# Kernel optimization log

Hardware: AMD Instinct MI355X
Metric: run time of the kernel (lower is better)

Reference implementation:

```python
import jax, jax.numpy as jnp
import numpy as np

BLOCK = 32          # per_1x32 microscaling block size along K
FP4_MAX = 6.0       # largest magnitude representable in e2m1
FP4_EMAX = 2.0      # exponent of largest fp4 binade (4..6)


def _quant_dequant_mxfp4(x):
    """Simulate MXFP4 (e2m1 elements, shared power-of-two E8M0 scale per 1x32
    block along the last dim): quantize then dequantize. x: [..., K], K % 32 == 0."""
    shape = x.shape
    xb = x.reshape(*shape[:-1], shape[-1] // BLOCK, BLOCK)
    amax = jnp.max(jnp.abs(xb), axis=-1, keepdims=True)
    # shared scale: 2^(floor(log2(amax)) - emax) so the block max lands in the top binade
    exp = jnp.floor(jnp.log2(jnp.maximum(amax, jnp.finfo(x.dtype).tiny))) - FP4_EMAX
    scale = jnp.where(amax > 0, jnp.exp2(exp), jnp.ones_like(amax))
    q = jnp.clip(xb / scale, -FP4_MAX, FP4_MAX)
    aq = jnp.abs(q)
    # e2m1 ulp: 0.5 on [0,2), 1 on [2,4), 2 on [4,6]
    lsb = jnp.where(aq < 2.0, 0.5, jnp.where(aq < 4.0, 1.0, 2.0))
    qr = jnp.round(q / lsb) * lsb  # round-to-nearest-even onto the fp4 grid
    return (qr * scale).reshape(shape)


def setup_inputs() -> dict:
    key = jax.random.key(0)
    k1, k2, k3 = jax.random.split(key, 3)
    B, S, K, N = 4, 2048, 2048, 2048
    inp = jax.random.normal(k1, (B, S, K), dtype=jnp.float32)
    weight = jax.random.normal(k2, (N, K), dtype=jnp.float32) * (1.0 / np.sqrt(K))
    bias = jax.random.normal(k3, (N,), dtype=jnp.float32) * 0.02
    return {"input": inp, "weight": weight, "bias": bias}


def reference(input, weight, bias):
    # both activation and weight are fake-quantized to MXFP4 per 1x32 blocks
    # along the contraction (in_features) dim, then a standard GEMM + bias.
    orig_shape = input.shape
    a = _quant_dequant_mxfp4(input.reshape(-1, orig_shape[-1]))  # [M, K]
    w = _quant_dequant_mxfp4(weight)                              # [N, K]
    out = jnp.einsum("mk,nk->mn", a, w) + bias
    return out.reshape(*orig_shape[:-1], weight.shape[0])
```

## Files before the change

### kernel.cpp

```cpp
#include <hip/hip_runtime.h>
#include <cstdint>


#define BM 128
#define BN 128
#define BK 128

typedef float floatx4 __attribute__((ext_vector_type(4)));
typedef int intx8 __attribute__((ext_vector_type(8)));

#define GLOBAL_AS __attribute__((address_space(1)))
#define LDS_AS __attribute__((address_space(3)))


__device__ __forceinline__ int enc1(float x, float inv) {
    float q = x * inv;
    q = fminf(fmaxf(q, -6.0f), 6.0f);
    int s = (int)(__float_as_uint(q) >> 31) << 3;
    float aq = fabsf(q);
    float ilsb = aq < 2.0f ? 2.0f : (aq < 4.0f ? 1.0f : 0.5f);
    float lsb  = aq < 2.0f ? 0.5f : (aq < 4.0f ? 1.0f : 2.0f);
    float ar = rintf(aq * ilsb) * lsb;
    int c;
    if (ar < 2.0f)      c = (int)(ar * 2.0f);
    else if (ar < 4.0f) c = 2 + (int)ar;
    else                c = 4 + (int)(ar * 0.5f);
    return c | s;
}

__global__ void quant_mxfp4_v4(const float* __restrict__ A, uint8_t* __restrict__ Aq,
                               uint8_t* __restrict__ AscT,
                               const float* __restrict__ W, uint8_t* __restrict__ Wq,
                               uint8_t* __restrict__ WscT,
                               long na4, long ntot4, int s4, long Mr, long Nr) {
    long t = (long)blockIdx.x * 256 + threadIdx.x;
    if (t >= ntot4) return;
    const float* src; uint8_t* dq; uint8_t* ds; long idx; long rows;
    if (t < na4) { src = A; dq = Aq; ds = AscT; idx = t; rows = Mr; }
    else         { src = W; dq = Wq; ds = WscT; idx = t - na4; rows = Nr; }

    float4 f = ((const float4*)src)[idx];
    float amax = fmaxf(fmaxf(fabsf(f.x), fabsf(f.y)),
                       fmaxf(fabsf(f.z), fabsf(f.w)));
    amax = fmaxf(amax, __shfl_xor(amax, 1));
    amax = fmaxf(amax, __shfl_xor(amax, 2));
    amax = fmaxf(amax, __shfl_xor(amax, 4));

    int ebits = (int)((__float_as_uint(amax) >> 23) & 0xff);
    int sb;
    float inv;
    if (amax > 0.0f) {
        sb = ebits - 2; if (sb < 0) sb = 0;
        inv = __uint_as_float((unsigned)((256 - ebits) & 255) << 23);
    } else {
        sb = 127;
        inv = 0.0f;
    }

    int c0 = enc1(f.x, inv), c1 = enc1(f.y, inv);
    int c2 = enc1(f.z, inv), c3 = enc1(f.w, inv);
    ((unsigned short*)dq)[idx] =
        (unsigned short)(c0 | (c1 << 4) | (c2 << 8) | (c3 << 12));
    if ((idx & 7) == 0) {
        long m  = idx >> s4;
        int  kb = (int)((idx & ((1L << s4) - 1)) >> 3);
        ds[(size_t)kb * rows + m] = (uint8_t)sb;
    }
}


__global__ __launch_bounds__(256, 4) void gemm_fp4_v4(
        const uint8_t* __restrict__ Aq, const uint8_t* __restrict__ AscT,
        const uint8_t* __restrict__ Wq, const uint8_t* __restrict__ WscT,
        const float* __restrict__ bias, float* __restrict__ C,
        int M, int N, int K) {
    __shared__ __align__(16) uint8_t sA[2][BM * 64];
    __shared__ __align__(16) uint8_t sB[2][BN * 64];
    __shared__ __align__(16) uint8_t sSA[2][4 * 128];
    __shared__ __align__(16) uint8_t sSB[2][4 * 128];

    const int tid = threadIdx.x;
    const int lane = tid & 63;
    const int w = tid >> 6;
    const int wr = w >> 1;
    const int wc = w & 1;
    const int row16 = lane & 15;
    const int quad = lane >> 4;

    const int id = blockIdx.x;
    const int g = id & 7, h = id >> 3;
    const int by = g + 8 * (h & 7);
    const int bx = h >> 3;
    const int m0 = by * BM;
    const int n0 = bx * BN;
    const int KB2 = K >> 1;
    const int NT = K / BK;

    const int rA = wr * 64 + row16;
    const int rB = wc * 64 + row16;

    floatx4 acc[4][4];
#pragma unroll
    for (int i = 0; i < 4; i++)
#pragma unroll
        for (int j = 0; j < 4; j++) acc[i][j] = (floatx4){0.f, 0.f, 0.f, 0.f};

    auto stage = [&](int tt) {
        const int bb = tt & 1;
        const int kb = tt * 64;
#pragma unroll
        for (int it = 0; it < 2; ++it) {
            int idx = it * 256 + tid;
            int row = idx >> 2, c = idx & 3;
            const uint8_t* src = Aq + (size_t)(m0 + row) * KB2 + kb + c * 16;
            __builtin_amdgcn_global_load_lds((GLOBAL_AS void*)src,
                (LDS_AS void*)(&sA[bb][idx * 16]), 16, 0, 0);
        }
#pragma unroll
        for (int it = 0; it < 2; ++it) {
            int idx = it * 256 + tid;
            int row = idx >> 2, c = idx & 3;
            const uint8_t* src = Wq + (size_t)(n0 + row) * KB2 + kb + c * 16;
            __builtin_amdgcn_global_load_lds((GLOBAL_AS void*)src,
                (LDS_AS void*)(&sB[bb][idx * 16]), 16, 0, 0);
        }
        if (tid < 128) {
            int kbi = tid >> 5, moff = (tid & 31) * 4;
            const uint8_t* src = AscT + (size_t)(4 * tt + kbi) * M + m0 + moff;
            __builtin_amdgcn_global_load_lds((GLOBAL_AS void*)src,
                (LDS_AS void*)(&sSA[bb][tid * 4]), 4, 0, 0);
        } else {
            int tw = tid - 128;
            int kbi = tw >> 5, noff = (tw & 31) * 4;
            const uint8_t* src = WscT + (size_t)(4 * tt + kbi) * N + n0 + noff;
            __builtin_amdgcn_global_load_lds((GLOBAL_AS void*)src,
                (LDS_AS void*)(&sSB[bb][tw * 4]), 4, 0, 0);
        }
    };

    stage(0);
    stage(1);
    asm volatile("s_waitcnt vmcnt(5)" ::: "memory");
    __builtin_amdgcn_sched_barrier(0);
    __builtin_amdgcn_s_barrier();

    for (int t = 0; t < NT; ++t) {
        const int p = t & 1;
        const uint8_t* pa = sA[p];
        const uint8_t* pb = sB[p];

        int4 afr[4], bfr[4];
        int sab[4], swb[4];
#pragma unroll
        for (int ni = 0; ni < 4; ++ni) {
            int r = rB + ni * 16;
            bfr[ni] = *(const int4*)(pb + r * 64 + quad * 16);
            swb[ni] = (int)sSB[p][quad * 128 + wc * 64 + ni * 16 + row16];
        }
#pragma unroll
        for (int mi = 0; mi < 4; ++mi) {
            int r = rA + mi * 16;
            afr[mi] = *(const int4*)(pa + r * 64 + quad * 16);
            sab[mi] = (int)sSA[p][quad * 128 + wr * 64 + mi * 16 + row16];
        }

        asm volatile("s_waitcnt lgkmcnt(0)" ::: "memory");
        __builtin_amdgcn_sched_barrier(0);
        __builtin_amdgcn_s_barrier();

        if (t + 2 < NT) stage(t + 2);

        __builtin_amdgcn_s_setprio(1);
#pragma unroll
        for (int mi = 0; mi < 4; ++mi) {
            intx8 a8 = {afr[mi].x, afr[mi].y, afr[mi].z, afr[mi].w, 0, 0, 0, 0};
#pragma unroll
            for (int ni = 0; ni < 4; ++ni) {
                intx8 b8 = {bfr[ni].x, bfr[ni].y, bfr[ni].z, bfr[ni].w, 0, 0, 0, 0};
                acc[mi][ni] = __builtin_amdgcn_mfma_scale_f32_16x16x128_f8f6f4(
                    a8, b8, acc[mi][ni], 4, 4, 0, sab[mi], 0, swb[ni]);
            }
        }
        __builtin_amdgcn_s_setprio(0);

        if (t < NT - 1) {
            if (t + 2 < NT) asm volatile("s_waitcnt vmcnt(5)" ::: "memory");
            else            asm volatile("s_waitcnt vmcnt(0)" ::: "memory");
            __builtin_amdgcn_sched_barrier(0);
            __builtin_amdgcn_s_barrier();
        }
    }

#pragma unroll
    for (int ni = 0; ni < 4; ++ni) {
        int n = n0 + wc * 64 + ni * 16 + row16;
        float bv = bias[n];
#pragma unroll
        for (int mi = 0; mi < 4; ++mi) {
            int mbase = m0 + wr * 64 + mi * 16 + quad * 4;
#pragma unroll
            for (int r = 0; r < 4; ++r) {
                C[(size_t)(mbase + r) * N + n] = acc[mi][ni][r] + bv;
            }
        }
    }
}


extern "C" void kernel_launch(void* const* d_in, const int* in_sizes, int n_in,
                              void* d_out, int out_size, void* d_ws, size_t ws_size,
                              hipStream_t stream) {
    const float* inp  = (const float*)d_in[0];
    const float* wgt  = (const float*)d_in[1];
    const float* bias = (const float*)d_in[2];
    float* out = (float*)d_out;

    const int N = in_sizes[2];
    const int K = in_sizes[1] / N;
    const long M = (long)in_sizes[0] / K;

    uint8_t* Aq4  = (uint8_t*)d_ws;
    uint8_t* Wq4  = Aq4 + (size_t)M * K / 2;
    uint8_t* AscT = Wq4 + (size_t)N * K / 2;
    uint8_t* WscT = AscT + (size_t)M * K / 32;

    int s4 = 0;
    while ((1 << s4) < (K >> 2)) ++s4;

    long na4   = (long)M * K / 4;
    long ntot4 = na4 + (long)N * K / 4;
    quant_mxfp4_v4<<<dim3((ntot4 + 255) / 256), dim3(256), 0, stream>>>(
        inp, Aq4, AscT, wgt, Wq4, WscT, na4, ntot4, s4, M, (long)N);

    dim3 grid((N / BN) * (int)(M / BM));
    gemm_fp4_v4<<<grid, dim3(256), 0, stream>>>(
        Aq4, AscT, Wq4, WscT, bias, out, (int)M, N, K);
}
```

Before: 156.7 us.

## Enlarge GEMM tile to 256x128 with 512 threads, triple-buffer LDS, split-phase loads

The FP4 GEMM moves from a 128x128 to a 256x128 block tile with 8 waves, and from double to triple LDS buffering. Each k-step is split into two MFMA phases, each preceded by its own A-fragment reads, and the prefetch of tile t+2 is split so A is issued in the first phase and B plus scales in the second, interleaving global-to-LDS loads with compute. This halves the grid and increases reuse of each B tile. In exchange it adds extra barriers per iteration, raises LDS use per block, which may lower occupancy, and reworks the block-index swizzle for the new grid shape.

```diff
diff --git a/kernel.cpp b/kernel.cpp
--- a/kernel.cpp
+++ b/kernel.cpp
@@ -2,9 +2,10 @@
 #include <cstdint>
 
 
-#define BM 128
+#define BM 256
 #define BN 128
 #define BK 128
+#define NBUF 3
 
 typedef float floatx4 __attribute__((ext_vector_type(4)));
 typedef int intx8 __attribute__((ext_vector_type(8)));
@@ -69,15 +70,15 @@
 }
 
 
-__global__ __launch_bounds__(256, 4) void gemm_fp4_v4(
+__global__ __launch_bounds__(512, 4) void gemm_fp4_v5(
         const uint8_t* __restrict__ Aq, const uint8_t* __restrict__ AscT,
         const uint8_t* __restrict__ Wq, const uint8_t* __restrict__ WscT,
         const float* __restrict__ bias, float* __restrict__ C,
         int M, int N, int K) {
-    __shared__ __align__(16) uint8_t sA[2][BM * 64];
-    __shared__ __align__(16) uint8_t sB[2][BN * 64];
-    __shared__ __align__(16) uint8_t sSA[2][4 * 128];
-    __shared__ __align__(16) uint8_t sSB[2][4 * 128];
+    __shared__ __align__(16) uint8_t sA[NBUF][BM * 64];
+    __shared__ __align__(16) uint8_t sB[NBUF][BN * 64];
+    __shared__ __align__(16) uint8_t sSA[NBUF][4 * BM];
+    __shared__ __align__(16) uint8_t sSB[NBUF][4 * BN];
 
     const int tid = threadIdx.x;
     const int lane = tid & 63;
@@ -89,8 +90,8 @@
 
     const int id = blockIdx.x;
     const int g = id & 7, h = id >> 3;
-    const int by = g + 8 * (h & 7);
-    const int bx = h >> 3;
+    const int by = g + 8 * (h & 3);
+    const int bx = h >> 2;
     const int m0 = by * BM;
     const int n0 = bx * BN;
     const int KB2 = K >> 1;
@@ -105,74 +106,76 @@
 #pragma unroll
         for (int j = 0; j < 4; j++) acc[i][j] = (floatx4){0.f, 0.f, 0.f, 0.f};
 
-    auto stage = [&](int tt) {
-        const int bb = tt & 1;
+    auto stageA = [&](int tt) {
+        const int bb = tt % NBUF;
         const int kb = tt * 64;
 #pragma unroll
         for (int it = 0; it < 2; ++it) {
-            int idx = it * 256 + tid;
+            int idx = it * 512 + tid;
             int row = idx >> 2, c = idx & 3;
             const uint8_t* src = Aq + (size_t)(m0 + row) * KB2 + kb + c * 16;
             __builtin_amdgcn_global_load_lds((GLOBAL_AS void*)src,
                 (LDS_AS void*)(&sA[bb][idx * 16]), 16, 0, 0);
         }
-#pragma unroll
-        for (int it = 0; it < 2; ++it) {
-            int idx = it * 256 + tid;
-            int row = idx >> 2, c = idx & 3;
+    };
+    auto stageB = [&](int tt) {
+        const int bb = tt % NBUF;
+        const int kb = tt * 64;
+        {
+            int row = tid >> 2, c = tid & 3;
             const uint8_t* src = Wq + (size_t)(n0 + row) * KB2 + kb + c * 16;
             __builtin_amdgcn_global_load_lds((GLOBAL_AS void*)src,
-                (LDS_AS void*)(&sB[bb][idx * 16]), 16, 0, 0);
-        }
-        if (tid < 128) {
-            int kbi = tid >> 5, moff = (tid & 31) * 4;
+                (LDS_AS void*)(&sB[bb][tid * 16]), 16, 0, 0);
+        }
+        if (tid >= 256) {
+            int local = tid - 256;
+            int kbi = local >> 6, moff = (local & 63) * 4;
             const uint8_t* src = AscT + (size_t)(4 * tt + kbi) * M + m0 + moff;
             __builtin_amdgcn_global_load_lds((GLOBAL_AS void*)src,
-                (LDS_AS void*)(&sSA[bb][tid * 4]), 4, 0, 0);
-        } else {
-            int tw = tid - 128;
-            int kbi = tw >> 5, noff = (tw & 31) * 4;
+                (LDS_AS void*)(&sSA[bb][local * 4]), 4, 0, 0);
+        } else if (tid < 128) {
+            int kbi = tid >> 5, noff = (tid & 31) * 4;
             const uint8_t* src = WscT + (size_t)(4 * tt + kbi) * N + n0 + noff;
             __builtin_amdgcn_global_load_lds((GLOBAL_AS void*)src,
-                (LDS_AS void*)(&sSB[bb][tw * 4]), 4, 0, 0);
+                (LDS_AS void*)(&sSB[bb][tid * 4]), 4, 0, 0);
         }
     };
 
-    stage(0);
-    stage(1);
-    asm volatile("s_waitcnt vmcnt(5)" ::: "memory");
+    stageA(0); stageB(0);
+    if (NT > 1) { stageA(1); stageB(1); }
+    if (NT > 1) asm volatile("s_waitcnt vmcnt(3)" ::: "memory");
+    else        asm volatile("s_waitcnt vmcnt(0)" ::: "memory");
     __builtin_amdgcn_sched_barrier(0);
     __builtin_amdgcn_s_barrier();
 
     for (int t = 0; t < NT; ++t) {
-        const int p = t & 1;
+        const int p = t % NBUF;
         const uint8_t* pa = sA[p];
         const uint8_t* pb = sB[p];
 
-        int4 afr[4], bfr[4];
-        int sab[4], swb[4];
+        int4 bfr[4]; int swb[4];
+        int4 afr[2]; int sab[2];
 #pragma unroll
         for (int ni = 0; ni < 4; ++ni) {
             int r = rB + ni * 16;
             bfr[ni] = *(const int4*)(pb + r * 64 + quad * 16);
-            swb[ni] = (int)sSB[p][quad * 128 + wc * 64 + ni * 16 + row16];
-        }
-#pragma unroll
-        for (int mi = 0; mi < 4; ++mi) {
+            swb[ni] = (int)sSB[p][quad * BN + wc * 64 + ni * 16 + row16];
+        }
+#pragma unroll
+        for (int mi = 0; mi < 2; ++mi) {
             int r = rA + mi * 16;
             afr[mi] = *(const int4*)(pa + r * 64 + quad * 16);
-            sab[mi] = (int)sSA[p][quad * 128 + wr * 64 + mi * 16 + row16];
-        }
-
+            sab[mi] = (int)sSA[p][quad * BM + wr * 64 + mi * 16 + row16];
+        }
+        if (t + 2 < NT) stageA(t + 2);
+
+        __builtin_amdgcn_s_barrier();
         asm volatile("s_waitcnt lgkmcnt(0)" ::: "memory");
         __builtin_amdgcn_sched_barrier(0);
-        __builtin_amdgcn_s_barrier();
-
-        if (t + 2 < NT) stage(t + 2);
 
         __builtin_amdgcn_s_setprio(1);
 #pragma unroll
-        for (int mi = 0; mi < 4; ++mi) {
+        for (int mi = 0; mi < 2; ++mi) {
             intx8 a8 = {afr[mi].x, afr[mi].y, afr[mi].z, afr[mi].w, 0, 0, 0, 0};
 #pragma unroll
             for (int ni = 0; ni < 4; ++ni) {
@@ -182,13 +185,39 @@
             }
         }
         __builtin_amdgcn_s_setprio(0);
+        __builtin_amdgcn_s_barrier();
+
+#pragma unroll
+        for (int mi = 0; mi < 2; ++mi) {
+            int r = rA + (mi + 2) * 16;
+            afr[mi] = *(const int4*)(pa + r * 64 + quad * 16);
+            sab[mi] = (int)sSA[p][quad * BM + wr * 64 + (mi + 2) * 16 + row16];
+        }
+        if (t + 2 < NT) stageB(t + 2);
+
+        __builtin_amdgcn_s_barrier();
+        asm volatile("s_waitcnt lgkmcnt(0)" ::: "memory");
+        __builtin_amdgcn_sched_barrier(0);
+
+        __builtin_amdgcn_s_setprio(1);
+#pragma unroll
+        for (int mi = 0; mi < 2; ++mi) {
+            intx8 a8 = {afr[mi].x, afr[mi].y, afr[mi].z, afr[mi].w, 0, 0, 0, 0};
+#pragma unroll
+            for (int ni = 0; ni < 4; ++ni) {
+                intx8 b8 = {bfr[ni].x, bfr[ni].y, bfr[ni].z, bfr[ni].w, 0, 0, 0, 0};
+                acc[mi + 2][ni] = __builtin_amdgcn_mfma_scale_f32_16x16x128_f8f6f4(
+                    a8, b8, acc[mi + 2][ni], 4, 4, 0, sab[mi], 0, swb[ni]);
+            }
+        }
+        __builtin_amdgcn_s_setprio(0);
 
         if (t < NT - 1) {
-            if (t + 2 < NT) asm volatile("s_waitcnt vmcnt(5)" ::: "memory");
+            if (t + 2 < NT) asm volatile("s_waitcnt vmcnt(3)" ::: "memory");
             else            asm volatile("s_waitcnt vmcnt(0)" ::: "memory");
             __builtin_amdgcn_sched_barrier(0);
-            __builtin_amdgcn_s_barrier();
-        }
+        }
+        __builtin_amdgcn_s_barrier();
     }
 
 #pragma unroll
@@ -233,6 +262,6 @@
         inp, Aq4, AscT, wgt, Wq4, WscT, na4, ntot4, s4, M, (long)N);
 
     dim3 grid((N / BN) * (int)(M / BM));
-    gemm_fp4_v4<<<grid, dim3(256), 0, stream>>>(
+    gemm_fp4_v5<<<grid, dim3(512), 0, stream>>>(
         Aq4, AscT, Wq4, WscT, bias, out, (int)M, N, K);
 }
```

Measured after the change: 166.6 us. 6.4% more time.

## Switch GEMM to 32x32x64 scaled MFMA with swizzled LDS and direct scale loads

Applied to the files above, without the earlier changes.

Replaces the 16x16x128 scaled MFMA tiling with 32x32x64 MFMAs: each wave now computes 2x2 tiles of 32x32 and splits the 128-wide K step into two sub-steps. The global-to-LDS copy applies an XOR swizzle on 16-byte chunks so that fragment reads hit fewer LDS bank conflicts. Block scales are now read straight from global memory into registers instead of being staged through LDS. The wait and barrier logic is restructured so the vmcnt wait comes before the MFMAs, which may reduce overlap between loads and compute, and the per-lane global scale loads add latency inside the loop.

```diff
diff --git a/kernel.cpp b/kernel.cpp
--- a/kernel.cpp
+++ b/kernel.cpp
@@ -6,7 +6,7 @@
 #define BN 128
 #define BK 128
 
-typedef float floatx4 __attribute__((ext_vector_type(4)));
+typedef float floatx16 __attribute__((ext_vector_type(16)));
 typedef int intx8 __attribute__((ext_vector_type(8)));
 
 #define GLOBAL_AS __attribute__((address_space(1)))
@@ -69,23 +69,21 @@
 }
 
 
-__global__ __launch_bounds__(256, 4) void gemm_fp4_v4(
+__global__ __launch_bounds__(256, 4) void gemm_fp4_v6(
         const uint8_t* __restrict__ Aq, const uint8_t* __restrict__ AscT,
         const uint8_t* __restrict__ Wq, const uint8_t* __restrict__ WscT,
         const float* __restrict__ bias, float* __restrict__ C,
         int M, int N, int K) {
     __shared__ __align__(16) uint8_t sA[2][BM * 64];
     __shared__ __align__(16) uint8_t sB[2][BN * 64];
-    __shared__ __align__(16) uint8_t sSA[2][4 * 128];
-    __shared__ __align__(16) uint8_t sSB[2][4 * 128];
 
     const int tid = threadIdx.x;
     const int lane = tid & 63;
     const int w = tid >> 6;
     const int wr = w >> 1;
     const int wc = w & 1;
-    const int row16 = lane & 15;
-    const int quad = lane >> 4;
+    const int row32 = lane & 31;
+    const int q2 = lane >> 5;
 
     const int id = blockIdx.x;
     const int g = id & 7, h = id >> 3;
@@ -96,14 +94,22 @@
     const int KB2 = K >> 1;
     const int NT = K / BK;
 
-    const int rA = wr * 64 + row16;
-    const int rB = wc * 64 + row16;
-
-    floatx4 acc[4][4];
-#pragma unroll
-    for (int i = 0; i < 4; i++)
-#pragma unroll
-        for (int j = 0; j < 4; j++) acc[i][j] = (floatx4){0.f, 0.f, 0.f, 0.f};
+    const int rA = wr * 64 + row32;
+    const int rB = wc * 64 + row32;
+    const int swz = (row32 >> 1) & 3;
+    const int off0 = ((0 * 2 + q2) ^ swz) * 16;
+    const int off1 = ((1 * 2 + q2) ^ swz) * 16;
+
+    const uint8_t* pScA = AscT + (size_t)q2 * M + m0 + wr * 64 + row32;
+    const uint8_t* pScB = WscT + (size_t)q2 * N + n0 + wc * 64 + row32;
+
+    floatx16 acc[2][2];
+#pragma unroll
+    for (int i = 0; i < 2; i++)
+#pragma unroll
+        for (int j = 0; j < 2; j++)
+#pragma unroll
+            for (int r = 0; r < 16; r++) acc[i][j][r] = 0.f;
 
     auto stage = [&](int tt) {
         const int bb = tt & 1;
@@ -112,7 +118,8 @@
         for (int it = 0; it < 2; ++it) {
             int idx = it * 256 + tid;
             int row = idx >> 2, c = idx & 3;
-            const uint8_t* src = Aq + (size_t)(m0 + row) * KB2 + kb + c * 16;
+            int gc = c ^ ((row >> 1) & 3);
+            const uint8_t* src = Aq + (size_t)(m0 + row) * KB2 + kb + gc * 16;
             __builtin_amdgcn_global_load_lds((GLOBAL_AS void*)src,
                 (LDS_AS void*)(&sA[bb][idx * 16]), 16, 0, 0);
         }
@@ -120,27 +127,16 @@
         for (int it = 0; it < 2; ++it) {
             int idx = it * 256 + tid;
             int row = idx >> 2, c = idx & 3;
-            const uint8_t* src = Wq + (size_t)(n0 + row) * KB2 + kb + c * 16;
+            int gc = c ^ ((row >> 1) & 3);
+            const uint8_t* src = Wq + (size_t)(n0 + row) * KB2 + kb + gc * 16;
             __builtin_amdgcn_global_load_lds((GLOBAL_AS void*)src,
                 (LDS_AS void*)(&sB[bb][idx * 16]), 16, 0, 0);
         }
-        if (tid < 128) {
-            int kbi = tid >> 5, moff = (tid & 31) * 4;
-            const uint8_t* src = AscT + (size_t)(4 * tt + kbi) * M + m0 + moff;
-            __builtin_amdgcn_global_load_lds((GLOBAL_AS void*)src,
-                (LDS_AS void*)(&sSA[bb][tid * 4]), 4, 0, 0);
-        } else {
-            int tw = tid - 128;
-            int kbi = tw >> 5, noff = (tw & 31) * 4;
-            const uint8_t* src = WscT + (size_t)(4 * tt + kbi) * N + n0 + noff;
-            __builtin_amdgcn_global_load_lds((GLOBAL_AS void*)src,
-                (LDS_AS void*)(&sSB[bb][tw * 4]), 4, 0, 0);
-        }
     };
 
     stage(0);
     stage(1);
-    asm volatile("s_waitcnt vmcnt(5)" ::: "memory");
+    asm volatile("s_waitcnt vmcnt(4)" ::: "memory");
     __builtin_amdgcn_sched_barrier(0);
     __builtin_amdgcn_s_barrier();
 
@@ -149,19 +145,22 @@
         const uint8_t* pa = sA[p];
         const uint8_t* pb = sB[p];
 
-        int4 afr[4], bfr[4];
-        int sab[4], swb[4];
-#pragma unroll
-        for (int ni = 0; ni < 4; ++ni) {
-            int r = rB + ni * 16;
-            bfr[ni] = *(const int4*)(pb + r * 64 + quad * 16);
-            swb[ni] = (int)sSB[p][quad * 128 + wc * 64 + ni * 16 + row16];
-        }
-#pragma unroll
-        for (int mi = 0; mi < 4; ++mi) {
-            int r = rA + mi * 16;
-            afr[mi] = *(const int4*)(pa + r * 64 + quad * 16);
-            sab[mi] = (int)sSA[p][quad * 128 + wr * 64 + mi * 16 + row16];
+        int sa[2][2], sb[2][2];
+#pragma unroll
+        for (int ks = 0; ks < 2; ++ks)
+#pragma unroll
+            for (int i = 0; i < 2; ++i) {
+                sa[ks][i] = (int)pScA[(size_t)(2 * ks) * M + i * 32];
+                sb[ks][i] = (int)pScB[(size_t)(2 * ks) * N + i * 32];
+            }
+
+        int4 fa[2][2], fb[2][2];
+#pragma unroll
+        for (int i = 0; i < 2; ++i) {
+            fa[0][i] = *(const int4*)(pa + (rA + i * 32) * 64 + off0);
+            fa[1][i] = *(const int4*)(pa + (rA + i * 32) * 64 + off1);
+            fb[0][i] = *(const int4*)(pb + (rB + i * 32) * 64 + off0);
+            fb[1][i] = *(const int4*)(pb + (rB + i * 32) * 64 + off1);
         }
 
         asm volatile("s_waitcnt lgkmcnt(0)" ::: "memory");
@@ -170,37 +169,47 @@
 
         if (t + 2 < NT) stage(t + 2);
 
+        if (t + 2 < NT) asm volatile("s_waitcnt vmcnt(4)" ::: "memory");
+        else            asm volatile("s_waitcnt vmcnt(0)" ::: "memory");
+        __builtin_amdgcn_sched_barrier(0);
+
         __builtin_amdgcn_s_setprio(1);
 #pragma unroll
-        for (int mi = 0; mi < 4; ++mi) {
-            intx8 a8 = {afr[mi].x, afr[mi].y, afr[mi].z, afr[mi].w, 0, 0, 0, 0};
-#pragma unroll
-            for (int ni = 0; ni < 4; ++ni) {
-                intx8 b8 = {bfr[ni].x, bfr[ni].y, bfr[ni].z, bfr[ni].w, 0, 0, 0, 0};
-                acc[mi][ni] = __builtin_amdgcn_mfma_scale_f32_16x16x128_f8f6f4(
-                    a8, b8, acc[mi][ni], 4, 4, 0, sab[mi], 0, swb[ni]);
-            }
+        for (int ks = 0; ks < 2; ++ks) {
+            intx8 a0, a1, b0, b1;
+            a0[0] = fa[ks][0].x; a0[1] = fa[ks][0].y; a0[2] = fa[ks][0].z; a0[3] = fa[ks][0].w;
+            a1[0] = fa[ks][1].x; a1[1] = fa[ks][1].y; a1[2] = fa[ks][1].z; a1[3] = fa[ks][1].w;
+            b0[0] = fb[ks][0].x; b0[1] = fb[ks][0].y; b0[2] = fb[ks][0].z; b0[3] = fb[ks][0].w;
+            b1[0] = fb[ks][1].x; b1[1] = fb[ks][1].y; b1[2] = fb[ks][1].z; b1[3] = fb[ks][1].w;
+#pragma unroll
+            for (int z = 4; z < 8; ++z) { a0[z] = 0; a1[z] = 0; b0[z] = 0; b1[z] = 0; }
+            acc[0][0] = __builtin_amdgcn_mfma_scale_f32_32x32x64_f8f6f4(
+                a0, b0, acc[0][0], 4, 4, 0, sa[ks][0], 0, sb[ks][0]);
+            acc[0][1] = __builtin_amdgcn_mfma_scale_f32_32x32x64_f8f6f4(
+                a0, b1, acc[0][1], 4, 4, 0, sa[ks][0], 0, sb[ks][1]);
+            acc[1][0] = __builtin_amdgcn_mfma_scale_f32_32x32x64_f8f6f4(
+                a1, b0, acc[1][0], 4, 4, 0, sa[ks][1], 0, sb[ks][0]);
+            acc[1][1] = __builtin_amdgcn_mfma_scale_f32_32x32x64_f8f6f4(
+                a1, b1, acc[1][1], 4, 4, 0, sa[ks][1], 0, sb[ks][1]);
         }
         __builtin_amdgcn_s_setprio(0);
-
-        if (t < NT - 1) {
-            if (t + 2 < NT) asm volatile("s_waitcnt vmcnt(5)" ::: "memory");
-            else            asm volatile("s_waitcnt vmcnt(0)" ::: "memory");
-            __builtin_amdgcn_sched_barrier(0);
-            __builtin_amdgcn_s_barrier();
-        }
-    }
-
-#pragma unroll
-    for (int ni = 0; ni < 4; ++ni) {
-        int n = n0 + wc * 64 + ni * 16 + row16;
+        __builtin_amdgcn_s_barrier();
+
+        pScA += (size_t)4 * M;
+        pScB += (size_t)4 * N;
+    }
+
+#pragma unroll
+    for (int j = 0; j < 2; ++j) {
+        int n = n0 + wc * 64 + j * 32 + row32;
         float bv = bias[n];
 #pragma unroll
-        for (int mi = 0; mi < 4; ++mi) {
-            int mbase = m0 + wr * 64 + mi * 16 + quad * 4;
-#pragma unroll
-            for (int r = 0; r < 4; ++r) {
-                C[(size_t)(mbase + r) * N + n] = acc[mi][ni][r] + bv;
+        for (int i = 0; i < 2; ++i) {
+            int mb = m0 + wr * 64 + i * 32 + 4 * q2;
+#pragma unroll
+            for (int r = 0; r < 16; ++r) {
+                int m = mb + (r & 3) + 8 * (r >> 2);
+                C[(size_t)m * N + n] = acc[i][j][r] + bv;
             }
         }
     }
@@ -233,6 +242,6 @@
         inp, Aq4, AscT, wgt, Wq4, WscT, na4, ntot4, s4, M, (long)N);
 
     dim3 grid((N / BN) * (int)(M / BM));
-    gemm_fp4_v4<<<grid, dim3(256), 0, stream>>>(
+    gemm_fp4_v6<<<grid, dim3(256), 0, stream>>>(
         Aq4, AscT, Wq4, WscT, bias, out, (int)M, N, K);
 }
```

New measurement: 153.1 us. 2.3% less time.
